# Kernel tuning notes

Hardware: AMD Instinct MI355X
Metric: run time of the kernel (lower is better)

The kernel has to match this reference:

```python
import jax, jax.numpy as jnp
import numpy as np

B, N, C = 2, 4096, 512
NUM_HEADS = 8
HEAD_DIM = C // NUM_HEADS
SCALE = HEAD_DIM ** -0.5
THETA = 10000.0


def setup_inputs() -> dict:
    key = jax.random.key(0)
    ks = jax.random.split(key, 5)
    x = jax.random.normal(ks[0], (B, N, C), dtype=jnp.float32)
    Wqkv = jax.random.normal(ks[1], (3 * C, C), dtype=jnp.float32) * 0.02
    bqkv = jax.random.normal(ks[2], (3 * C,), dtype=jnp.float32) * 0.02
    Wproj = jax.random.normal(ks[3], (C, C), dtype=jnp.float32) * 0.02
    bproj = jax.random.normal(ks[4], (C,), dtype=jnp.float32) * 0.02
    return {"x": x, "Wqkv": Wqkv, "bqkv": bqkv, "Wproj": Wproj, "bproj": bproj}


def _rope(x, seq_len, head_dim):
    # x: [B, H, N, head_dim]; interleaved rotary embedding
    freqs = 1.0 / THETA ** (jnp.arange(0, head_dim, 2, dtype=jnp.float32) / head_dim)  # [hd/2]
    t = jnp.arange(seq_len, dtype=jnp.float32)
    freqs_cis = jnp.outer(t, freqs)                      # [N, hd/2]
    sin_f = jnp.sin(freqs_cis)
    cos_f = jnp.cos(freqs_cis)
    x_even = x[..., ::2]                                 # [B, H, N, hd/2]
    x_odd = x[..., 1::2]
    rot = jnp.stack(
        [x_even * cos_f - x_odd * sin_f,
         x_even * sin_f + x_odd * cos_f],
        axis=-1,
    )                                                    # [B, H, N, hd/2, 2]
    return rot.reshape(x.shape)


def reference(x, Wqkv, bqkv, Wproj, bproj):
    b, n, c = x.shape
    # fused QKV projection: y = x @ W.T + b
    qkv = x @ Wqkv.T + bqkv                              # [B, N, 3C]
    qkv = qkv.reshape(b, n, 3, NUM_HEADS, HEAD_DIM)
    qkv = jnp.transpose(qkv, (2, 0, 3, 1, 4))            # [3, B, H, N, hd]
    q, k, v = qkv[0], qkv[1], qkv[2]
    q = _rope(q, n, HEAD_DIM)
    k = _rope(k, n, HEAD_DIM)
    attn = jnp.einsum('bhqd,bhkd->bhqk', q, k) * SCALE   # [B, H, N, N]
    attn = jax.nn.softmax(attn, axis=-1)
    out = jnp.einsum('bhqk,bhkd->bhqd', attn, v)         # [B, H, N, hd]
    out = jnp.transpose(out, (0, 2, 1, 3)).reshape(b, n, c)
    return out @ Wproj.T + bproj
```

## Files before the change

### kernel.cpp

```cpp
#include <hip/hip_runtime.h>
#include <hip/hip_bf16.h>
#include <stdint.h>

#define B_ 2
#define N_ 4096
#define C_ 512
#define H_ 8
#define D_ 64
#define M_ (B_*N_)
#define K3_ (3*C_)

typedef __attribute__((ext_vector_type(8)))  short short8;
typedef __attribute__((ext_vector_type(4)))  float f32x4;
typedef __attribute__((ext_vector_type(16))) float f32x16;

static __device__ __forceinline__ unsigned short f2bf(float f) {
  union { float f; unsigned u; } cv; cv.f = f;
  unsigned r = cv.u + 0x7fffu + ((cv.u >> 16) & 1u);
  return (unsigned short)(r >> 16);
}
static __device__ __forceinline__ float bf2f(short x) {
  union { unsigned u; float f; } cv;
  cv.u = ((unsigned)(unsigned short)x) << 16;
  return cv.f;
}
static __device__ __forceinline__ float fexp2(float x) {
#if __has_builtin(__builtin_amdgcn_exp2f)
  return __builtin_amdgcn_exp2f(x);
#else
  return exp2f(x);
#endif
}
static __device__ __forceinline__ unsigned cvt_pk_bf16(float a, float b) {
  unsigned r;
  asm("v_cvt_pk_bf16_f32 %0, %1, %2" : "=v"(r) : "v"(a), "v"(b));
  return r;
}
static __device__ __forceinline__ void gload_lds16(const void* g, void* l) {
  __builtin_amdgcn_global_load_lds((const __attribute__((address_space(1))) unsigned*)g,
                                   (__attribute__((address_space(3))) unsigned*)l, 16, 0, 0);
}
static __device__ __forceinline__ f32x16 zero16() {
  f32x16 z;
#pragma unroll
  for (int i = 0; i < 16; i++) z[i] = 0.f;
  return z;
}

__global__ void cast_f2b(const float* __restrict__ in, short* __restrict__ out, int n4) {
  int i = blockIdx.x * blockDim.x + threadIdx.x;
  if (i >= n4) return;
  float4 v = ((const float4*)in)[i];
  short4 o;
  o.x = (short)f2bf(v.x); o.y = (short)f2bf(v.y);
  o.z = (short)f2bf(v.z); o.w = (short)f2bf(v.w);
  ((short4*)out)[i] = o;
}

__global__ void rope_table(float2* __restrict__ tab) {
  int i = blockIdx.x * blockDim.x + threadIdx.x;
  if (i >= N_ * 32) return;
  int p = i & 31, n = i >> 5;
  float freq = exp2f(-((float)(2 * p) / 64.0f) * 13.287712379549449f);
  float ang = (float)n * freq;
  float s, c;
  sincosf(ang, &s, &c);
  float2 r; r.x = c; r.y = s;
  tab[i] = r;
}

__global__ void rope_apply(const short* __restrict__ qkvb, const float2* __restrict__ tab,
                           short* __restrict__ Qf, short* __restrict__ Kf) {
  int idx = blockIdx.x * blockDim.x + threadIdx.x;
  if (idx >= 2 * M_ * 64) return;
  int lane  = idx & 63;
  int f     = (idx >> 6) & 3;
  int nblk  = (idx >> 8) & 127;
  int h     = (idx >> 15) & 7;
  int b     = (idx >> 18) & 1;
  int tk    = idx >> 19;
  int c = lane & 31, hi = lane >> 5;
  int n = nblk * 32 + c;
  int d0 = f * 16 + hi * 8;
  short8 v = *(const short8*)(qkvb + (size_t)(b * N_ + n) * K3_ + tk * C_ + h * D_ + d0);
  const float2* tp = tab + n * 32 + (d0 >> 1);
  float sc = (tk == 0) ? 0.18033688011112042f : 1.0f;
  short8 w;
#pragma unroll
  for (int j = 0; j < 4; j++) {
    float e = bf2f(v[2 * j]), o = bf2f(v[2 * j + 1]);
    float2 cs = tp[j];
    float e2 = (e * cs.x - o * cs.y) * sc;
    float o2 = (e * cs.y + o * cs.x) * sc;
    w[2 * j] = (short)f2bf(e2);
    w[2 * j + 1] = (short)f2bf(o2);
  }
  short* dst = (tk ? Kf : Qf) + (((size_t)((b * H_ + h) * 128 + nblk) * 4 + f) * 512) + lane * 8;
  *(short8*)dst = w;
}

__global__ void vtrans(const short* __restrict__ qkvb, short* __restrict__ Vf) {
  __shared__ short tile[32][72];
  int bh = blockIdx.x;
  int kblk = blockIdx.y;
  int b = bh >> 3, h = bh & 7;
  int t = threadIdx.x;
  int n0 = kblk * 32;
  {
    int row = t >> 3, c8 = t & 7;
    short8 v = *(const short8*)(qkvb + (size_t)(b * N_ + n0 + row) * K3_ + 2 * C_ + h * D_ + c8 * 8);
    *(short8*)&tile[row][c8 * 8] = v;
  }
  __syncthreads();
  {
    int frag = t >> 6, lane = t & 63;
    int hi = lane >> 5, c = lane & 31;
    int g = frag & 1, dblk = frag >> 1;
    short8 w;
#pragma unroll
    for (int j = 0; j < 8; j++) w[j] = tile[g * 16 + hi * 8 + j][dblk * 32 + c];
    *(short8*)(Vf + ((size_t)(bh * 128 + kblk) * 4 + frag) * 512 + lane * 8) = w;
  }
}

template<int OUTF32>
__global__ __launch_bounds__(256) void gemm_bt(const short* __restrict__ A, const short* __restrict__ Bw,
                                               const float* __restrict__ bias, void* __restrict__ Cout,
                                               int M, int Nout, int K) {
  __shared__ short As[128 * 32];
  __shared__ short Bs[128 * 32];
  int t = threadIdx.x, lane = t & 63, w = t >> 6, wr = w >> 1, wc = w & 1;
  int tM = blockIdx.x * 128, tN = blockIdx.y * 128;
  int lrow = lane & 15, lhi = lane >> 4;
  f32x4 acc[4][4];
#pragma unroll
  for (int fm = 0; fm < 4; fm++)
#pragma unroll
    for (int fn = 0; fn < 4; fn++)
#pragma unroll
      for (int r = 0; r < 4; r++) acc[fm][fn][r] = 0.f;

  int srow = t >> 2, sq = (t & 3) * 8;
  const short* Ag0 = A  + (size_t)(tM + srow) * K + sq;
  const short* Ag1 = A  + (size_t)(tM + 64 + srow) * K + sq;
  const short* Bg0 = Bw + (size_t)(tN + srow) * K + sq;
  const short* Bg1 = Bw + (size_t)(tN + 64 + srow) * K + sq;
  short* Al0 = As + t * 8;          short* Al1 = As + 2048 + t * 8;
  short* Bl0 = Bs + t * 8;          short* Bl1 = Bs + 2048 + t * 8;

  for (int k0 = 0; k0 < K; k0 += 32) {
    gload_lds16(Ag0 + k0, Al0);
    gload_lds16(Ag1 + k0, Al1);
    gload_lds16(Bg0 + k0, Bl0);
    gload_lds16(Bg1 + k0, Bl1);
    __syncthreads();
    short8 af[4], bfr[4];
#pragma unroll
    for (int f = 0; f < 4; f++) {
      af[f]  = *(const short8*)(As + (wr * 64 + f * 16 + lrow) * 32 + lhi * 8);
      bfr[f] = *(const short8*)(Bs + (wc * 64 + f * 16 + lrow) * 32 + lhi * 8);
    }
#pragma unroll
    for (int fm = 0; fm < 4; fm++)
#pragma unroll
      for (int fn = 0; fn < 4; fn++)
        acc[fm][fn] = __builtin_amdgcn_mfma_f32_16x16x32_bf16(af[fm], bfr[fn], acc[fm][fn], 0, 0, 0);
    __syncthreads();
  }

#pragma unroll
  for (int fn = 0; fn < 4; fn++) {
    int col = tN + wc * 64 + fn * 16 + lrow;
    float bv = bias[col];
#pragma unroll
    for (int fm = 0; fm < 4; fm++) {
      int row0 = tM + wr * 64 + fm * 16 + lhi * 4;
#pragma unroll
      for (int r = 0; r < 4; r++) {
        float v = acc[fm][fn][r] + bv;
        if (OUTF32) ((float*)Cout)[(size_t)(row0 + r) * Nout + col] = v;
        else        ((short*)Cout)[(size_t)(row0 + r) * Nout + col] = (short)f2bf(v);
      }
    }
  }
}

__global__ __launch_bounds__(256, 4) void attn(const short* __restrict__ Qf, const short* __restrict__ Kf,
                                               const short* __restrict__ Vf,
                                               float* __restrict__ Op, float* __restrict__ lp) {
  int bh = blockIdx.x;
  int ch = blockIdx.z;
  int wv = threadIdx.x >> 6, lane = threadIdx.x & 63;
  int c = lane & 31, hi = lane >> 5;
  int q0 = blockIdx.y * 128 + wv * 32;
  const int nkb = N_ / 64;
  int kb0 = ch * nkb;

  const short* Qb = Qf + ((size_t)(bh * 128 + (q0 >> 5)) * 4) * 512 + lane * 8;
  const short* Kb = Kf + ((size_t)(bh * 128 + kb0) * 4) * 512 + lane * 8;
  const short* Vb = Vf + ((size_t)(bh * 128 + kb0) * 4) * 512 + lane * 8;

  short8 qf4[4];
#pragma unroll
  for (int f = 0; f < 4; f++) qf4[f] = *(const short8*)(Qb + f * 512);

  f32x16 o0 = zero16(), o1 = zero16();
  float lsum = 0.f;

  short8 kf[4];
#pragma unroll
  for (int f = 0; f < 4; f++) kf[f] = *(const short8*)(Kb + f * 512);

  for (int it = 0; it < nkb; it++) {
    const short* Vt0 = Vb + (size_t)it * 2048;
    short8 vf00 = *(const short8*)(Vt0);
    short8 vf10 = *(const short8*)(Vt0 + 512);
    short8 vf01 = *(const short8*)(Vt0 + 1024);
    short8 vf11 = *(const short8*)(Vt0 + 1536);

    __builtin_amdgcn_s_setprio(1);
    f32x16 st = zero16();
#pragma unroll
    for (int f = 0; f < 4; f++)
      st = __builtin_amdgcn_mfma_f32_32x32x16_bf16(kf[f], qf4[f], st, 0, 0, 0);
    __builtin_amdgcn_s_setprio(0);

    const short* Kn = Kb + (size_t)((it + 1 < nkb) ? it + 1 : 0) * 2048;
    short8 kfn[4];
#pragma unroll
    for (int f = 0; f < 4; f++) kfn[f] = *(const short8*)(Kn + f * 512);

    float ls = 0.f;
    unsigned cpk[8];
#pragma unroll
    for (int q2 = 0; q2 < 4; q2++) {
      float e0 = fexp2(st[4 * q2]),     e1 = fexp2(st[4 * q2 + 1]);
      float e2 = fexp2(st[4 * q2 + 2]), e3 = fexp2(st[4 * q2 + 3]);
      ls += (e0 + e1) + (e2 + e3);
      cpk[2 * q2]     = cvt_pk_bf16(e0, e1);
      cpk[2 * q2 + 1] = cvt_pk_bf16(e2, e3);
    }
    lsum += ls;

    unsigned w00 = cpk[0], w02 = cpk[2];
    asm volatile("v_permlane32_swap_b32 %0, %1" : "+v"(w00), "+v"(w02));
    unsigned w01 = cpk[1], w03 = cpk[3];
    asm volatile("v_permlane32_swap_b32 %0, %1" : "+v"(w01), "+v"(w03));
    unsigned w10 = cpk[4], w12 = cpk[6];
    asm volatile("v_permlane32_swap_b32 %0, %1" : "+v"(w10), "+v"(w12));
    unsigned w11 = cpk[5], w13 = cpk[7];
    asm volatile("v_permlane32_swap_b32 %0, %1" : "+v"(w11), "+v"(w13));

    union { unsigned u[4]; short8 s; } u0, u1;
    u0.u[0] = w00; u0.u[1] = w01; u0.u[2] = w02; u0.u[3] = w03;
    u1.u[0] = w10; u1.u[1] = w11; u1.u[2] = w12; u1.u[3] = w13;

    __builtin_amdgcn_s_setprio(1);
    o0 = __builtin_amdgcn_mfma_f32_32x32x16_bf16(u0.s, vf00, o0, 0, 0, 0);
    o0 = __builtin_amdgcn_mfma_f32_32x32x16_bf16(u1.s, vf10, o0, 0, 0, 0);
    o1 = __builtin_amdgcn_mfma_f32_32x32x16_bf16(u0.s, vf01, o1, 0, 0, 0);
    o1 = __builtin_amdgcn_mfma_f32_32x32x16_bf16(u1.s, vf11, o1, 0, 0, 0);
    __builtin_amdgcn_s_setprio(0);

#pragma unroll
    for (int f = 0; f < 4; f++) kf[f] = kfn[f];
  }

  float lt = lsum + __shfl_xor(lsum, 32);
  if (hi == 0) lp[((size_t)ch * 16 + bh) * N_ + q0 + c] = lt;
  float* obase = Op + ((size_t)ch * 16 + bh) * N_ * D_;
#pragma unroll
  for (int r = 0; r < 16; r++) {
    int ql = (r & 3) + 8 * (r >> 2) + 4 * hi;
    int n = q0 + ql;
    obase[(size_t)n * D_ + c]      = o0[r];
    obase[(size_t)n * D_ + 32 + c] = o1[r];
  }
}

__global__ void combine(const float* __restrict__ Op, const float* __restrict__ lp,
                        short* __restrict__ AO) {
  int i = blockIdx.x * blockDim.x + threadIdx.x;
  if (i >= 16 * N_ * 16) return;
  int d4 = i & 15, q = (i >> 4) & (N_ - 1), bh = i >> 16;
  size_t base = ((size_t)bh * N_ + q) * D_ + d4 * 4;
  const size_t chstride = (size_t)16 * N_ * D_;
  float4 a = *(const float4*)(Op + base);
  float4 b = *(const float4*)(Op + base + chstride);
  float l = lp[(size_t)bh * N_ + q] + lp[(size_t)16 * N_ + (size_t)bh * N_ + q];
  float inv = 1.0f / l;
  int bb = bh >> 3, h = bh & 7;
  short4 o;
  o.x = (short)f2bf((a.x + b.x) * inv);
  o.y = (short)f2bf((a.y + b.y) * inv);
  o.z = (short)f2bf((a.z + b.z) * inv);
  o.w = (short)f2bf((a.w + b.w) * inv);
  *(short4*)(AO + ((size_t)(bb * N_ + q)) * C_ + h * D_ + d4 * 4) = o;
}

extern "C" void kernel_launch(void* const* d_in, const int* in_sizes, int n_in,
                              void* d_out, int out_size, void* d_ws, size_t ws_size,
                              hipStream_t stream) {
  const float* x     = (const float*)d_in[0];
  const float* Wqkv  = (const float*)d_in[1];
  const float* bqkv  = (const float*)d_in[2];
  const float* Wproj = (const float*)d_in[3];
  const float* bproj = (const float*)d_in[4];
  float* out = (float*)d_out;
  char* ws = (char*)d_ws;

  const size_t off_wprjb = 0;
  const size_t off_tab   = 524288;
  const size_t off_q     = 1572864;
  const size_t off_k     = 9961472;
  const size_t off_vt    = 18350080;
  const size_t off_ao    = 26738688;
  const size_t off_xb    = 35127296;
  const size_t off_wqkvb = 43515904;
  const size_t off_qkvb  = 45088768;
  const size_t off_op    = 35127296;
  const size_t off_l     = 68681728;
  if (ws_size < 70254592) return;

  short* xb    = (short*)(ws + off_xb);
  short* wqkvb = (short*)(ws + off_wqkvb);
  short* wprjb = (short*)(ws + off_wprjb);
  short* qkvb  = (short*)(ws + off_qkvb);
  short* Qfp   = (short*)(ws + off_q);
  short* Kfp   = (short*)(ws + off_k);
  short* Vfp   = (short*)(ws + off_vt);
  short* AOp   = (short*)(ws + off_ao);
  float2* tab  = (float2*)(ws + off_tab);
  float* Opp   = (float*)(ws + off_op);
  float* lpp   = (float*)(ws + off_l);

  cast_f2b<<<dim3(4096), dim3(256), 0, stream>>>(x,     xb,    M_ * C_ / 4);
  cast_f2b<<<dim3(768),  dim3(256), 0, stream>>>(Wqkv,  wqkvb, K3_ * C_ / 4);
  cast_f2b<<<dim3(256),  dim3(256), 0, stream>>>(Wproj, wprjb, C_ * C_ / 4);
  rope_table<<<dim3(512), dim3(256), 0, stream>>>(tab);

  gemm_bt<0><<<dim3(64, 12), dim3(256), 0, stream>>>(xb, wqkvb, bqkv, qkvb, M_, K3_, C_);

  rope_apply<<<dim3(4096), dim3(256), 0, stream>>>(qkvb, tab, Qfp, Kfp);
  vtrans<<<dim3(16, 128), dim3(256), 0, stream>>>(qkvb, Vfp);

  attn<<<dim3(16, 32, 2), dim3(256), 0, stream>>>(Qfp, Kfp, Vfp, Opp, lpp);
  combine<<<dim3(4096), dim3(256), 0, stream>>>(Opp, lpp, AOp);

  gemm_bt<1><<<dim3(64, 4), dim3(256), 0, stream>>>(AOp, wprjb, bproj, (void*)out, M_, C_, C_);
}
```

Before: 152.8 us.

## Software-pipeline attention loop two-deep and merge small prep kernels

The attention inner loop is unrolled by two with ping-pong K/V register buffers. The QK MFMA for the next key block is issued before the exp/softmax and PV of the current block, and K/V loads are prefetched two blocks ahead. This is meant to overlap transcendental and permute work with matrix-core work and hide load latency. Separately, the three cast kernels and the rope table are merged into one launch, and rope_apply and vtrans into another, to cut launch overhead. The cost is more live registers in a kernel capped by launch_bounds(256,4), which could cause spills.

After: 246.7 us. 1.61x slower.

```diff
diff --git a/kernel.cpp b/kernel.cpp
--- a/kernel.cpp
+++ b/kernel.cpp
@@ -47,79 +47,95 @@
   return z;
 }
 
-__global__ void cast_f2b(const float* __restrict__ in, short* __restrict__ out, int n4) {
-  int i = blockIdx.x * blockDim.x + threadIdx.x;
-  if (i >= n4) return;
-  float4 v = ((const float4*)in)[i];
-  short4 o;
-  o.x = (short)f2bf(v.x); o.y = (short)f2bf(v.y);
-  o.z = (short)f2bf(v.z); o.w = (short)f2bf(v.w);
-  ((short4*)out)[i] = o;
-}
-
-__global__ void rope_table(float2* __restrict__ tab) {
-  int i = blockIdx.x * blockDim.x + threadIdx.x;
-  if (i >= N_ * 32) return;
-  int p = i & 31, n = i >> 5;
-  float freq = exp2f(-((float)(2 * p) / 64.0f) * 13.287712379549449f);
-  float ang = (float)n * freq;
-  float s, c;
-  sincosf(ang, &s, &c);
-  float2 r; r.x = c; r.y = s;
-  tab[i] = r;
-}
-
-__global__ void rope_apply(const short* __restrict__ qkvb, const float2* __restrict__ tab,
-                           short* __restrict__ Qf, short* __restrict__ Kf) {
-  int idx = blockIdx.x * blockDim.x + threadIdx.x;
-  if (idx >= 2 * M_ * 64) return;
-  int lane  = idx & 63;
-  int f     = (idx >> 6) & 3;
-  int nblk  = (idx >> 8) & 127;
-  int h     = (idx >> 15) & 7;
-  int b     = (idx >> 18) & 1;
-  int tk    = idx >> 19;
-  int c = lane & 31, hi = lane >> 5;
-  int n = nblk * 32 + c;
-  int d0 = f * 16 + hi * 8;
-  short8 v = *(const short8*)(qkvb + (size_t)(b * N_ + n) * K3_ + tk * C_ + h * D_ + d0);
-  const float2* tp = tab + n * 32 + (d0 >> 1);
-  float sc = (tk == 0) ? 0.18033688011112042f : 1.0f;
-  short8 w;
-#pragma unroll
-  for (int j = 0; j < 4; j++) {
-    float e = bf2f(v[2 * j]), o = bf2f(v[2 * j + 1]);
-    float2 cs = tp[j];
-    float e2 = (e * cs.x - o * cs.y) * sc;
-    float o2 = (e * cs.y + o * cs.x) * sc;
-    w[2 * j] = (short)f2bf(e2);
-    w[2 * j + 1] = (short)f2bf(o2);
-  }
-  short* dst = (tk ? Kf : Qf) + (((size_t)((b * H_ + h) * 128 + nblk) * 4 + f) * 512) + lane * 8;
-  *(short8*)dst = w;
-}
-
-__global__ void vtrans(const short* __restrict__ qkvb, short* __restrict__ Vf) {
+__global__ void prep(const float* __restrict__ x, const float* __restrict__ Wqkv,
+                     const float* __restrict__ Wproj,
+                     short* __restrict__ xb, short* __restrict__ wqkvb,
+                     short* __restrict__ wprjb, float2* __restrict__ tab) {
+  int blk = blockIdx.x, t = threadIdx.x;
+  if (blk < 4096) {
+    int i = blk * 256 + t;
+    float4 v = ((const float4*)x)[i];
+    short4 o;
+    o.x = (short)f2bf(v.x); o.y = (short)f2bf(v.y);
+    o.z = (short)f2bf(v.z); o.w = (short)f2bf(v.w);
+    ((short4*)xb)[i] = o;
+  } else if (blk < 4864) {
+    int i = (blk - 4096) * 256 + t;
+    float4 v = ((const float4*)Wqkv)[i];
+    short4 o;
+    o.x = (short)f2bf(v.x); o.y = (short)f2bf(v.y);
+    o.z = (short)f2bf(v.z); o.w = (short)f2bf(v.w);
+    ((short4*)wqkvb)[i] = o;
+  } else if (blk < 5120) {
+    int i = (blk - 4864) * 256 + t;
+    float4 v = ((const float4*)Wproj)[i];
+    short4 o;
+    o.x = (short)f2bf(v.x); o.y = (short)f2bf(v.y);
+    o.z = (short)f2bf(v.z); o.w = (short)f2bf(v.w);
+    ((short4*)wprjb)[i] = o;
+  } else {
+    int i = (blk - 5120) * 256 + t;
+    int p = i & 31, n = i >> 5;
+    float freq = exp2f(-((float)(2 * p) / 64.0f) * 13.287712379549449f);
+    float ang = (float)n * freq;
+    float s, c;
+    sincosf(ang, &s, &c);
+    float2 r; r.x = c; r.y = s;
+    tab[i] = r;
+  }
+}
+
+__global__ void rope_vt(const short* __restrict__ qkvb, const float2* __restrict__ tab,
+                        short* __restrict__ Qf, short* __restrict__ Kf,
+                        short* __restrict__ Vf) {
   __shared__ short tile[32][72];
-  int bh = blockIdx.x;
-  int kblk = blockIdx.y;
-  int b = bh >> 3, h = bh & 7;
-  int t = threadIdx.x;
-  int n0 = kblk * 32;
-  {
-    int row = t >> 3, c8 = t & 7;
-    short8 v = *(const short8*)(qkvb + (size_t)(b * N_ + n0 + row) * K3_ + 2 * C_ + h * D_ + c8 * 8);
-    *(short8*)&tile[row][c8 * 8] = v;
-  }
-  __syncthreads();
-  {
-    int frag = t >> 6, lane = t & 63;
-    int hi = lane >> 5, c = lane & 31;
-    int g = frag & 1, dblk = frag >> 1;
+  int blk = blockIdx.x, t = threadIdx.x;
+  if (blk < 4096) {
+    int idx = blk * 256 + t;
+    int lane  = idx & 63;
+    int f     = (idx >> 6) & 3;
+    int nblk  = (idx >> 8) & 127;
+    int h     = (idx >> 15) & 7;
+    int b     = (idx >> 18) & 1;
+    int tk    = idx >> 19;
+    int c = lane & 31, hi = lane >> 5;
+    int n = nblk * 32 + c;
+    int d0 = f * 16 + hi * 8;
+    short8 v = *(const short8*)(qkvb + (size_t)(b * N_ + n) * K3_ + tk * C_ + h * D_ + d0);
+    const float2* tp = tab + n * 32 + (d0 >> 1);
+    float sc = (tk == 0) ? 0.18033688011112042f : 1.0f;
     short8 w;
 #pragma unroll
-    for (int j = 0; j < 8; j++) w[j] = tile[g * 16 + hi * 8 + j][dblk * 32 + c];
-    *(short8*)(Vf + ((size_t)(bh * 128 + kblk) * 4 + frag) * 512 + lane * 8) = w;
+    for (int j = 0; j < 4; j++) {
+      float e = bf2f(v[2 * j]), o = bf2f(v[2 * j + 1]);
+      float2 cs = tp[j];
+      float e2 = (e * cs.x - o * cs.y) * sc;
+      float o2 = (e * cs.y + o * cs.x) * sc;
+      w[2 * j] = (short)f2bf(e2);
+      w[2 * j + 1] = (short)f2bf(o2);
+    }
+    short* dst = (tk ? Kf : Qf) + (((size_t)((b * H_ + h) * 128 + nblk) * 4 + f) * 512) + lane * 8;
+    *(short8*)dst = w;
+  } else {
+    int blk2 = blk - 4096;
+    int bh = blk2 >> 7, kblk = blk2 & 127;
+    int b = bh >> 3, h = bh & 7;
+    int n0 = kblk * 32;
+    {
+      int row = t >> 3, c8 = t & 7;
+      short8 v = *(const short8*)(qkvb + (size_t)(b * N_ + n0 + row) * K3_ + 2 * C_ + h * D_ + c8 * 8);
+      *(short8*)&tile[row][c8 * 8] = v;
+    }
+    __syncthreads();
+    {
+      int frag = t >> 6, lane = t & 63;
+      int hi = lane >> 5, c = lane & 31;
+      int g = frag & 1, dblk = frag >> 1;
+      short8 w;
+#pragma unroll
+      for (int j = 0; j < 8; j++) w[j] = tile[g * 16 + hi * 8 + j][dblk * 32 + c];
+      *(short8*)(Vf + ((size_t)(bh * 128 + kblk) * 4 + frag) * 512 + lane * 8) = w;
+    }
   }
 }
 
@@ -185,6 +201,51 @@
   }
 }
 
+static __device__ __forceinline__ void ld4(short8* dst, const short* p) {
+#pragma unroll
+  for (int f = 0; f < 4; f++) dst[f] = *(const short8*)(p + f * 512);
+}
+static __device__ __forceinline__ f32x16 qk4(const short8* k, const short8* q, const f32x16& z0) {
+  __builtin_amdgcn_s_setprio(1);
+  f32x16 st = __builtin_amdgcn_mfma_f32_32x32x16_bf16(k[0], q[0], z0, 0, 0, 0);
+  st = __builtin_amdgcn_mfma_f32_32x32x16_bf16(k[1], q[1], st, 0, 0, 0);
+  st = __builtin_amdgcn_mfma_f32_32x32x16_bf16(k[2], q[2], st, 0, 0, 0);
+  st = __builtin_amdgcn_mfma_f32_32x32x16_bf16(k[3], q[3], st, 0, 0, 0);
+  __builtin_amdgcn_s_setprio(0);
+  return st;
+}
+static __device__ __forceinline__ void soft_pv(const f32x16& st, const short8* v,
+                                               f32x16& o0, f32x16& o1, float& lsum) {
+  float ls = 0.f;
+  unsigned cpk[8];
+#pragma unroll
+  for (int q2 = 0; q2 < 4; q2++) {
+    float e0 = fexp2(st[4 * q2]),     e1 = fexp2(st[4 * q2 + 1]);
+    float e2 = fexp2(st[4 * q2 + 2]), e3 = fexp2(st[4 * q2 + 3]);
+    ls += (e0 + e1) + (e2 + e3);
+    cpk[2 * q2]     = cvt_pk_bf16(e0, e1);
+    cpk[2 * q2 + 1] = cvt_pk_bf16(e2, e3);
+  }
+  lsum += ls;
+  unsigned w00 = cpk[0], w02 = cpk[2];
+  asm volatile("v_permlane32_swap_b32 %0, %1" : "+v"(w00), "+v"(w02));
+  unsigned w01 = cpk[1], w03 = cpk[3];
+  asm volatile("v_permlane32_swap_b32 %0, %1" : "+v"(w01), "+v"(w03));
+  unsigned w10 = cpk[4], w12 = cpk[6];
+  asm volatile("v_permlane32_swap_b32 %0, %1" : "+v"(w10), "+v"(w12));
+  unsigned w11 = cpk[5], w13 = cpk[7];
+  asm volatile("v_permlane32_swap_b32 %0, %1" : "+v"(w11), "+v"(w13));
+  union { unsigned u[4]; short8 s; } u0, u1;
+  u0.u[0] = w00; u0.u[1] = w01; u0.u[2] = w02; u0.u[3] = w03;
+  u1.u[0] = w10; u1.u[1] = w11; u1.u[2] = w12; u1.u[3] = w13;
+  __builtin_amdgcn_s_setprio(1);
+  o0 = __builtin_amdgcn_mfma_f32_32x32x16_bf16(u0.s, v[0], o0, 0, 0, 0);
+  o0 = __builtin_amdgcn_mfma_f32_32x32x16_bf16(u1.s, v[1], o0, 0, 0, 0);
+  o1 = __builtin_amdgcn_mfma_f32_32x32x16_bf16(u0.s, v[2], o1, 0, 0, 0);
+  o1 = __builtin_amdgcn_mfma_f32_32x32x16_bf16(u1.s, v[3], o1, 0, 0, 0);
+  __builtin_amdgcn_s_setprio(0);
+}
+
 __global__ __launch_bounds__(256, 4) void attn(const short* __restrict__ Qf, const short* __restrict__ Kf,
                                                const short* __restrict__ Vf,
                                                float* __restrict__ Op, float* __restrict__ lp) {
@@ -201,69 +262,27 @@
   const short* Vb = Vf + ((size_t)(bh * 128 + kb0) * 4) * 512 + lane * 8;
 
   short8 qf4[4];
-#pragma unroll
-  for (int f = 0; f < 4; f++) qf4[f] = *(const short8*)(Qb + f * 512);
-
-  f32x16 o0 = zero16(), o1 = zero16();
+  ld4(qf4, Qb);
+
+  const f32x16 z0 = zero16();
+  f32x16 o0 = z0, o1 = z0;
   float lsum = 0.f;
 
-  short8 kf[4];
-#pragma unroll
-  for (int f = 0; f < 4; f++) kf[f] = *(const short8*)(Kb + f * 512);
-
-  for (int it = 0; it < nkb; it++) {
-    const short* Vt0 = Vb + (size_t)it * 2048;
-    short8 vf00 = *(const short8*)(Vt0);
-    short8 vf10 = *(const short8*)(Vt0 + 512);
-    short8 vf01 = *(const short8*)(Vt0 + 1024);
-    short8 vf11 = *(const short8*)(Vt0 + 1536);
-
-    __builtin_amdgcn_s_setprio(1);
-    f32x16 st = zero16();
-#pragma unroll
-    for (int f = 0; f < 4; f++)
-      st = __builtin_amdgcn_mfma_f32_32x32x16_bf16(kf[f], qf4[f], st, 0, 0, 0);
-    __builtin_amdgcn_s_setprio(0);
-
-    const short* Kn = Kb + (size_t)((it + 1 < nkb) ? it + 1 : 0) * 2048;
-    short8 kfn[4];
-#pragma unroll
-    for (int f = 0; f < 4; f++) kfn[f] = *(const short8*)(Kn + f * 512);
-
-    float ls = 0.f;
-    unsigned cpk[8];
-#pragma unroll
-    for (int q2 = 0; q2 < 4; q2++) {
-      float e0 = fexp2(st[4 * q2]),     e1 = fexp2(st[4 * q2 + 1]);
-      float e2 = fexp2(st[4 * q2 + 2]), e3 = fexp2(st[4 * q2 + 3]);
-      ls += (e0 + e1) + (e2 + e3);
-      cpk[2 * q2]     = cvt_pk_bf16(e0, e1);
-      cpk[2 * q2 + 1] = cvt_pk_bf16(e2, e3);
-    }
-    lsum += ls;
-
-    unsigned w00 = cpk[0], w02 = cpk[2];
-    asm volatile("v_permlane32_swap_b32 %0, %1" : "+v"(w00), "+v"(w02));
-    unsigned w01 = cpk[1], w03 = cpk[3];
-    asm volatile("v_permlane32_swap_b32 %0, %1" : "+v"(w01), "+v"(w03));
-    unsigned w10 = cpk[4], w12 = cpk[6];
-    asm volatile("v_permlane32_swap_b32 %0, %1" : "+v"(w10), "+v"(w12));
-    unsigned w11 = cpk[5], w13 = cpk[7];
-    asm volatile("v_permlane32_swap_b32 %0, %1" : "+v"(w11), "+v"(w13));
-
-    union { unsigned u[4]; short8 s; } u0, u1;
-    u0.u[0] = w00; u0.u[1] = w01; u0.u[2] = w02; u0.u[3] = w03;
-    u1.u[0] = w10; u1.u[1] = w11; u1.u[2] = w12; u1.u[3] = w13;
-
-    __builtin_amdgcn_s_setprio(1);
-    o0 = __builtin_amdgcn_mfma_f32_32x32x16_bf16(u0.s, vf00, o0, 0, 0, 0);
-    o0 = __builtin_amdgcn_mfma_f32_32x32x16_bf16(u1.s, vf10, o0, 0, 0, 0);
-    o1 = __builtin_amdgcn_mfma_f32_32x32x16_bf16(u0.s, vf01, o1, 0, 0, 0);
-    o1 = __builtin_amdgcn_mfma_f32_32x32x16_bf16(u1.s, vf11, o1, 0, 0, 0);
-    __builtin_amdgcn_s_setprio(0);
-
-#pragma unroll
-    for (int f = 0; f < 4; f++) kf[f] = kfn[f];
+  short8 kA[4], kB[4], vA[4], vB[4];
+  ld4(kA, Kb);
+  ld4(kB, Kb + 2048);
+  ld4(vA, Vb);
+  f32x16 stA = qk4(kA, qf4, z0);
+
+  for (int it = 0; it < nkb; it += 2) {
+    f32x16 stB = qk4(kB, qf4, z0);
+    ld4(kA, Kb + (size_t)((it + 2) & 63) * 2048);
+    ld4(vB, Vb + (size_t)((it + 1) & 63) * 2048);
+    soft_pv(stA, vA, o0, o1, lsum);
+    stA = qk4(kA, qf4, z0);
+    ld4(kB, Kb + (size_t)((it + 3) & 63) * 2048);
+    ld4(vA, Vb + (size_t)((it + 2) & 63) * 2048);
+    soft_pv(stB, vB, o0, o1, lsum);
   }
 
   float lt = lsum + __shfl_xor(lsum, 32);
@@ -334,15 +353,11 @@
   float* Opp   = (float*)(ws + off_op);
   float* lpp   = (float*)(ws + off_l);
 
-  cast_f2b<<<dim3(4096), dim3(256), 0, stream>>>(x,     xb,    M_ * C_ / 4);
-  cast_f2b<<<dim3(768),  dim3(256), 0, stream>>>(Wqkv,  wqkvb, K3_ * C_ / 4);
-  cast_f2b<<<dim3(256),  dim3(256), 0, stream>>>(Wproj, wprjb, C_ * C_ / 4);
-  rope_table<<<dim3(512), dim3(256), 0, stream>>>(tab);
+  prep<<<dim3(5632), dim3(256), 0, stream>>>(x, Wqkv, Wproj, xb, wqkvb, wprjb, tab);
 
   gemm_bt<0><<<dim3(64, 12), dim3(256), 0, stream>>>(xb, wqkvb, bqkv, qkvb, M_, K3_, C_);
 
-  rope_apply<<<dim3(4096), dim3(256), 0, stream>>>(qkvb, tab, Qfp, Kfp);
-  vtrans<<<dim3(16, 128), dim3(256), 0, stream>>>(qkvb, Vfp);
+  rope_vt<<<dim3(6144), dim3(256), 0, stream>>>(qkvb, tab, Qfp, Kfp, Vfp);
 
   attn<<<dim3(16, 32, 2), dim3(256), 0, stream>>>(Qfp, Kfp, Vfp, Opp, lpp);
   combine<<<dim3(4096), dim3(256), 0, stream>>>(Opp, lpp, AOp);
```
